# Kernel tuning notes

Measured on AMD Instinct MI355X. Metric: run time of the kernel, lower is better.

## Reference

```python
import jax, jax.numpy as jnp
import numpy as np

NUM_USERS = 100000
NUM_ITEMS = 50000
EMB_DIM = 128
N_EDGES = 1600000
BATCH = 16384
L_USER = (0, 1, 2)


def setup_inputs() -> dict:
    key = jax.random.key(0)
    k1, k2, k3, k4, k5, k6 = jax.random.split(key, 6)
    users = jax.random.randint(k1, (BATCH,), 0, NUM_USERS)
    items = jax.random.randint(k2, (BATCH,), 0, NUM_ITEMS)
    edge_src = jax.random.randint(k3, (N_EDGES,), 0, NUM_USERS)
    edge_dst = jax.random.randint(k4, (N_EDGES,), 0, NUM_USERS)
    # nn.Parameter init: normal(mean=0, std=0.01)
    user_emb = jax.random.normal(k5, (NUM_USERS, EMB_DIM), dtype=jnp.float32) * 0.01
    item_emb = jax.random.normal(k6, (NUM_ITEMS, EMB_DIM), dtype=jnp.float32) * 0.01
    return {"users": users, "items": items, "edge_src": edge_src,
            "edge_dst": edge_dst, "user_emb": user_emb, "item_emb": item_emb}


def social_conv(edge_src, edge_dst, h):
    # DGL copy_u -> mean aggregation over social (user-user) edges
    msgs = h[edge_src]  # [E, D] gather
    agg = jax.ops.segment_sum(msgs, edge_dst, num_segments=NUM_USERS)  # [N, D]
    deg = jax.ops.segment_sum(jnp.ones_like(edge_dst, dtype=h.dtype), edge_dst,
                              num_segments=NUM_USERS)  # [N]
    return agg / jnp.maximum(deg, 1.0)[:, None]


def reference(users, items, edge_src, edge_dst, user_emb, item_emb):
    g1 = social_conv(edge_src, edge_dst, user_emb)
    g2 = social_conv(edge_src, edge_dst, g1)
    final_user = jnp.zeros_like(user_emb)
    if 0 in L_USER:
        final_user = final_user + user_emb
    if 1 in L_USER:
        final_user = final_user + g1
    if 2 in L_USER:
        final_user = final_user + g2
    latest_user = final_user[users]   # [B, D]
    latest_item = item_emb[items]     # [B, D]
    predict = jax.nn.sigmoid(jnp.sum(latest_user * latest_item, axis=1))  # [B]
    return predict, latest_user, latest_item
```

## Files before the change

kernel.cpp:

```cpp
#include <hip/hip_runtime.h>
#include <math.h>

#define NUM_USERS 100000
#define NUM_ITEMS 50000
#define EMB_D 128
#define N_EDGES 1600000
#define BATCH 16384

#define NBINS 782
#define CHUNK 8192
#define NCHUNKS 196
#define CELL 40
#define CAP 64
#define BINSZ (NCHUNKS * CELL)

#define CVT_BLOCKS 3125

#define FP8_SCALE 512.0f
#define FP8_INV   (1.0f / 512.0f)

typedef unsigned int u32;
typedef unsigned char u8;
typedef float f32x2 __attribute__((ext_vector_type(2)));

__device__ __forceinline__ long long g18row(int u) {
    return (long long)(u >> 7) * BINSZ + (long long)(u & 127) * 32;
}

__global__ void prep_kernel(const float* __restrict__ in, u32* __restrict__ outp,
                            const int* __restrict__ edge_src, const int* __restrict__ edge_dst,
                            u32* __restrict__ coarse, u8* __restrict__ cellcnt) {
    __shared__ int cnt2[NBINS];
    int blk = blockIdx.x;
    int tid = threadIdx.x;
    if (blk >= NCHUNKS) {
        long long bbase = (long long)(blk - NCHUNKS) * 1024;
        float4 a[4];
        #pragma unroll
        for (int g = 0; g < 4; g++) a[g] = ((const float4*)in)[bbase + g * 256 + tid];
        #pragma unroll
        for (int g = 0; g < 4; g++) {
            int r = __builtin_amdgcn_cvt_pk_fp8_f32(a[g].x * FP8_SCALE, a[g].y * FP8_SCALE, 0, false);
            r = __builtin_amdgcn_cvt_pk_fp8_f32(a[g].z * FP8_SCALE, a[g].w * FP8_SCALE, r, true);
            outp[bbase + g * 256 + tid] = (u32)r;
        }
        return;
    }
    long long c0 = (long long)blk * CHUNK;
    int n = (int)min((long long)CHUNK, (long long)N_EDGES - c0);
    for (int i = tid; i < NBINS; i += 256) cnt2[i] = 0;
    __syncthreads();
    int n4 = n >> 2;
    const int4* d4p = (const int4*)(edge_dst + c0);
    const int4* s4p = (const int4*)(edge_src + c0);
    for (int i = tid; i < n4; i += 256) {
        int4 d = d4p[i];
        int4 s = s4p[i];
        int dd[4] = {d.x, d.y, d.z, d.w};
        int ss[4] = {s.x, s.y, s.z, s.w};
        #pragma unroll
        for (int k = 0; k < 4; k++) {
            int b = dd[k] >> 7;
            int idx = atomicAdd(&cnt2[b], 1);
            if (idx < CELL)
                coarse[(long long)b * BINSZ + blk * CELL + idx] =
                    ((u32)ss[k] << 7) | (u32)(dd[k] & 127);
        }
    }
    __syncthreads();
    for (int i = tid; i < NBINS; i += 256)
        cellcnt[(long long)blk * NBINS + i] = (u8)min(cnt2[i], CELL);
}

__global__ void binagg_kernel(u32* __restrict__ coarse, const u8* __restrict__ cellcnt,
                              const u32* __restrict__ tab32,
                              int* __restrict__ srt, int* __restrict__ counts) {
    __shared__ int cur[128];
    __shared__ int stage[128 * 65];
    int b = blockIdx.x;
    int tid = threadIdx.x;
    if (tid < 128) cur[tid] = 0;
    __syncthreads();
    long long cb = (long long)b * BINSZ;
    for (int i = tid; i < BINSZ; i += 512) {
        int cell = i / CELL;
        int slot = i - cell * CELL;
        if (slot < (int)cellcnt[(long long)cell * NBINS + b]) {
            u32 p = coarse[cb + i];
            int dl = (int)(p & 127u);
            int pos = atomicAdd(&cur[dl], 1);
            if (pos < CAP) stage[dl * 65 + pos] = (int)(p >> 7);
        }
    }
    __syncthreads();
    int binBase = b << 7;
    int wv = tid >> 6;
    int lane = tid & 63;
    int dlane = lane & 31;
    int hi = lane >> 5;
    for (int dl = wv; dl < 128; dl += 8) {
        int user = binBase + dl;
        if (user >= NUM_USERS) continue;
        int cnt = cur[dl];
        int cl = min(cnt, CAP);
        int sbase = dl * 65;
        float4 acc = make_float4(0.f, 0.f, 0.f, 0.f);
        int j = 0;
        for (; j + 16 <= cl; j += 16) {
            int rr[8];
            #pragma unroll
            for (int k = 0; k < 8; k++) {
                int s0 = stage[sbase + j + 2 * k];
                int s1 = stage[sbase + j + 2 * k + 1];
                rr[k] = hi ? s1 : s0;
            }
            u32 pp[8];
            #pragma unroll
            for (int k = 0; k < 8; k++) pp[k] = tab32[(long long)rr[k] * 32 + dlane];
            #pragma unroll
            for (int k = 0; k < 8; k++) {
                f32x2 d0 = __builtin_amdgcn_cvt_pk_f32_fp8((int)pp[k], false);
                f32x2 d1 = __builtin_amdgcn_cvt_pk_f32_fp8((int)pp[k], true);
                acc.x += d0.x; acc.y += d0.y; acc.z += d1.x; acc.w += d1.y;
            }
        }
        if (j < cl) {
            int rr[8]; float ww[8];
            #pragma unroll
            for (int k = 0; k < 8; k++) {
                int i0 = min(j + 2 * k, cl - 1);
                int i1 = min(j + 2 * k + 1, cl - 1);
                int s0 = stage[sbase + i0];
                int s1 = stage[sbase + i1];
                rr[k] = hi ? s1 : s0;
                ww[k] = ((j + 2 * k + hi) < cl) ? 1.0f : 0.0f;
            }
            u32 pp[8];
            #pragma unroll
            for (int k = 0; k < 8; k++) pp[k] = tab32[(long long)rr[k] * 32 + dlane];
            #pragma unroll
            for (int k = 0; k < 8; k++) {
                f32x2 d0 = __builtin_amdgcn_cvt_pk_f32_fp8((int)pp[k], false);
                f32x2 d1 = __builtin_amdgcn_cvt_pk_f32_fp8((int)pp[k], true);
                acc.x += d0.x * ww[k]; acc.y += d0.y * ww[k];
                acc.z += d1.x * ww[k]; acc.w += d1.y * ww[k];
            }
        }
        acc.x += __shfl_xor(acc.x, 32, 64);
        acc.y += __shfl_xor(acc.y, 32, 64);
        acc.z += __shfl_xor(acc.z, 32, 64);
        acc.w += __shfl_xor(acc.w, 32, 64);
        float inv = 1.0f / fmaxf((float)cnt, 1.0f);
        int enc = __builtin_amdgcn_cvt_pk_fp8_f32(acc.x * inv, acc.y * inv, 0, false);
        enc = __builtin_amdgcn_cvt_pk_fp8_f32(acc.z * inv, acc.w * inv, enc, true);
        if (lane < 32) coarse[g18row(user) + dlane] = (u32)enc;
        srt[(long long)user * CAP + lane] = stage[sbase + lane];
        if (lane == 0) counts[user] = cnt;
    }
}

__global__ void final_kernel(const int* __restrict__ users, const int* __restrict__ items,
                             const float* __restrict__ user_emb, const float* __restrict__ item_emb,
                             const u32* __restrict__ g18, const int* __restrict__ counts,
                             const int* __restrict__ srt,
                             float* __restrict__ out_predict, float* __restrict__ out_lu,
                             float* __restrict__ out_li) {
    int b = (blockIdx.x * blockDim.x + threadIdx.x) >> 6;
    int lane = threadIdx.x & 63;
    if (b >= BATCH) return;
    b = __builtin_amdgcn_readfirstlane(b);
    int u = users[b];
    int it = items[b];
    int cnt = counts[u];
    int cl = min(cnt, CAP);
    long long start = (long long)u * CAP;
    int dlane = lane & 31;
    int hi = lane >> 5;
    float4 acc = make_float4(0.f, 0.f, 0.f, 0.f);
    int j = 0;
    for (; j + 16 <= cl; j += 16) {
        int rr[8];
        #pragma unroll
        for (int k = 0; k < 8; k++) {
            int s0 = srt[start + j + 2 * k];
            int s1 = srt[start + j + 2 * k + 1];
            rr[k] = hi ? s1 : s0;
        }
        u32 pp[8];
        #pragma unroll
        for (int k = 0; k < 8; k++) pp[k] = g18[g18row(rr[k]) + dlane];
        #pragma unroll
        for (int k = 0; k < 8; k++) {
            f32x2 d0 = __builtin_amdgcn_cvt_pk_f32_fp8((int)pp[k], false);
            f32x2 d1 = __builtin_amdgcn_cvt_pk_f32_fp8((int)pp[k], true);
            acc.x += d0.x; acc.y += d0.y; acc.z += d1.x; acc.w += d1.y;
        }
    }
    if (j < cl) {
        int rr[8]; float ww[8];
        #pragma unroll
        for (int k = 0; k < 8; k++) {
            int i0 = min(j + 2 * k, cl - 1);
            int i1 = min(j + 2 * k + 1, cl - 1);
            int s0 = srt[start + i0];
            int s1 = srt[start + i1];
            rr[k] = hi ? s1 : s0;
            ww[k] = ((j + 2 * k + hi) < cl) ? 1.0f : 0.0f;
        }
        u32 pp[8];
        #pragma unroll
        for (int k = 0; k < 8; k++) pp[k] = g18[g18row(rr[k]) + dlane];
        #pragma unroll
        for (int k = 0; k < 8; k++) {
            f32x2 d0 = __builtin_amdgcn_cvt_pk_f32_fp8((int)pp[k], false);
            f32x2 d1 = __builtin_amdgcn_cvt_pk_f32_fp8((int)pp[k], true);
            acc.x += d0.x * ww[k]; acc.y += d0.y * ww[k];
            acc.z += d1.x * ww[k]; acc.w += d1.y * ww[k];
        }
    }
    acc.x += __shfl_xor(acc.x, 32, 64);
    acc.y += __shfl_xor(acc.y, 32, 64);
    acc.z += __shfl_xor(acc.z, 32, 64);
    acc.w += __shfl_xor(acc.w, 32, 64);
    float inv = (1.0f / fmaxf((float)cnt, 1.0f)) * FP8_INV;
    float4 ue = *(const float4*)(user_emb + (long long)u * EMB_D + dlane * 4);
    u32 a1p = g18[g18row(u) + dlane];
    f32x2 a0 = __builtin_amdgcn_cvt_pk_f32_fp8((int)a1p, false);
    f32x2 a1 = __builtin_amdgcn_cvt_pk_f32_fp8((int)a1p, true);
    float4 ie = *(const float4*)(item_emb + (long long)it * EMB_D + dlane * 4);
    float4 lu;
    lu.x = ue.x + a0.x * FP8_INV + acc.x * inv;
    lu.y = ue.y + a0.y * FP8_INV + acc.y * inv;
    lu.z = ue.z + a1.x * FP8_INV + acc.z * inv;
    lu.w = ue.w + a1.y * FP8_INV + acc.w * inv;
    if (lane < 32) {
        *(float4*)(out_lu + (long long)b * EMB_D + dlane * 4) = lu;
        *(float4*)(out_li + (long long)b * EMB_D + dlane * 4) = ie;
    }
    float dot = lu.x * ie.x + lu.y * ie.y + lu.z * ie.z + lu.w * ie.w;
    #pragma unroll
    for (int off = 16; off > 0; off >>= 1) dot += __shfl_down(dot, off, 64);
    if (lane == 0) out_predict[b] = 1.0f / (1.0f + expf(-dot));
}

extern "C" void kernel_launch(void* const* d_in, const int* in_sizes, int n_in,
                              void* d_out, int out_size, void* d_ws, size_t ws_size,
                              hipStream_t stream) {
    const int* users     = (const int*)d_in[0];
    const int* items     = (const int*)d_in[1];
    const int* edge_src  = (const int*)d_in[2];
    const int* edge_dst  = (const int*)d_in[3];
    const float* user_emb = (const float*)d_in[4];
    const float* item_emb = (const float*)d_in[5];

    const long long COARSE_U32 = (long long)NBINS * BINSZ;

    int* ws_i = (int*)d_ws;
    int* counts = ws_i;
    int* srt    = counts + 100352;
    u32* ue8    = (u32*)(srt + (long long)NUM_USERS * CAP);
    u32* coarse = ue8 + 3200000;
    u8*  cellcnt = (u8*)(coarse + COARSE_U32);

    float* out_predict = (float*)d_out;
    float* out_lu = out_predict + BATCH;
    float* out_li = out_lu + (long long)BATCH * EMB_D;

    prep_kernel<<<NCHUNKS + CVT_BLOCKS, 256, 0, stream>>>(
        user_emb, ue8, edge_src, edge_dst, coarse, cellcnt);

    binagg_kernel<<<NBINS, 512, 0, stream>>>(coarse, cellcnt, ue8, srt, counts);

    final_kernel<<<(BATCH + 3) / 4, 256, 0, stream>>>(
        users, items, user_emb, item_emb, coarse, counts, srt,
        out_predict, out_lu, out_li);
}
```

Measured before the change: 232.3 us.

## Stage edge partition cells in LDS with sentinels and write srt only for batch users

Splits the prep kernel into a separate fp8 conversion kernel (which also builds a bitmap of batch users) and a partition kernel that fills per-bin cells in LDS. Cells are pre-filled with a sentinel and then written to global memory as full uint4 rows. This removes the per-cell count array and the scattered 4-byte global writes, and lets binagg read coarse with vector loads and skip sentinels. binagg now writes the srt neighbour list only for users that appear in the batch, which cuts global write traffic. The cost is an extra memset and kernel launch, plus a partition kernel using about 128KB of dynamic LDS, which limits occupancy to one block per CU.

Measured after the change: 210.6 us. -9.4%, faster.

```diff
diff --git a/kernel.cpp b/kernel.cpp
--- a/kernel.cpp
+++ b/kernel.cpp
@@ -13,47 +13,61 @@
 #define CELL 40
 #define CAP 64
 #define BINSZ (NCHUNKS * CELL)
+#define SENT 0xFFFFFFFFu
 
 #define CVT_BLOCKS 3125
+#define BMAP_BLOCKS 64
 
 #define FP8_SCALE 512.0f
 #define FP8_INV   (1.0f / 512.0f)
 
 typedef unsigned int u32;
-typedef unsigned char u8;
 typedef float f32x2 __attribute__((ext_vector_type(2)));
 
 __device__ __forceinline__ long long g18row(int u) {
     return (long long)(u >> 7) * BINSZ + (long long)(u & 127) * 32;
 }
 
-__global__ void prep_kernel(const float* __restrict__ in, u32* __restrict__ outp,
-                            const int* __restrict__ edge_src, const int* __restrict__ edge_dst,
-                            u32* __restrict__ coarse, u8* __restrict__ cellcnt) {
-    __shared__ int cnt2[NBINS];
+__global__ void cvt_kernel(const float* __restrict__ in, u32* __restrict__ outp,
+                           const int* __restrict__ users, u32* __restrict__ bitmap) {
     int blk = blockIdx.x;
     int tid = threadIdx.x;
-    if (blk >= NCHUNKS) {
-        long long bbase = (long long)(blk - NCHUNKS) * 1024;
-        float4 a[4];
-        #pragma unroll
-        for (int g = 0; g < 4; g++) a[g] = ((const float4*)in)[bbase + g * 256 + tid];
-        #pragma unroll
-        for (int g = 0; g < 4; g++) {
-            int r = __builtin_amdgcn_cvt_pk_fp8_f32(a[g].x * FP8_SCALE, a[g].y * FP8_SCALE, 0, false);
-            r = __builtin_amdgcn_cvt_pk_fp8_f32(a[g].z * FP8_SCALE, a[g].w * FP8_SCALE, r, true);
-            outp[bbase + g * 256 + tid] = (u32)r;
+    if (blk >= CVT_BLOCKS) {
+        int i = (blk - CVT_BLOCKS) * 256 + tid;
+        if (i < BATCH) {
+            int u = users[i];
+            atomicOr(&bitmap[u >> 5], 1u << (u & 31));
         }
         return;
     }
+    long long bbase = (long long)blk * 1024;
+    float4 a[4];
+    #pragma unroll
+    for (int g = 0; g < 4; g++) a[g] = ((const float4*)in)[bbase + g * 256 + tid];
+    #pragma unroll
+    for (int g = 0; g < 4; g++) {
+        int r = __builtin_amdgcn_cvt_pk_fp8_f32(a[g].x * FP8_SCALE, a[g].y * FP8_SCALE, 0, false);
+        r = __builtin_amdgcn_cvt_pk_fp8_f32(a[g].z * FP8_SCALE, a[g].w * FP8_SCALE, r, true);
+        outp[bbase + g * 256 + tid] = (u32)r;
+    }
+}
+
+__global__ void part_kernel(const int* __restrict__ edge_src, const int* __restrict__ edge_dst,
+                            u32* __restrict__ coarse) {
+    extern __shared__ u32 sm[];
+    u32* cells = sm;
+    int* cnt2  = (int*)(sm + NBINS * CELL);
+    int blk = blockIdx.x;
+    int tid = threadIdx.x;
+    for (int i = tid; i < NBINS * CELL; i += 512) cells[i] = SENT;
+    for (int i = tid; i < NBINS; i += 512) cnt2[i] = 0;
+    __syncthreads();
     long long c0 = (long long)blk * CHUNK;
     int n = (int)min((long long)CHUNK, (long long)N_EDGES - c0);
-    for (int i = tid; i < NBINS; i += 256) cnt2[i] = 0;
-    __syncthreads();
     int n4 = n >> 2;
     const int4* d4p = (const int4*)(edge_dst + c0);
     const int4* s4p = (const int4*)(edge_src + c0);
-    for (int i = tid; i < n4; i += 256) {
+    for (int i = tid; i < n4; i += 512) {
         int4 d = d4p[i];
         int4 s = s4p[i];
         int dd[4] = {d.x, d.y, d.z, d.w};
@@ -63,17 +77,21 @@
             int b = dd[k] >> 7;
             int idx = atomicAdd(&cnt2[b], 1);
             if (idx < CELL)
-                coarse[(long long)b * BINSZ + blk * CELL + idx] =
-                    ((u32)ss[k] << 7) | (u32)(dd[k] & 127);
+                cells[b * CELL + idx] = ((u32)ss[k] << 7) | (u32)(dd[k] & 127);
         }
     }
     __syncthreads();
-    for (int i = tid; i < NBINS; i += 256)
-        cellcnt[(long long)blk * NBINS + i] = (u8)min(cnt2[i], CELL);
-}
-
-__global__ void binagg_kernel(u32* __restrict__ coarse, const u8* __restrict__ cellcnt,
-                              const u32* __restrict__ tab32,
+    const int I4 = NBINS * (CELL / 4);
+    for (int i4 = tid; i4 < I4; i4 += 512) {
+        int bin = i4 / (CELL / 4);
+        int off = i4 - bin * (CELL / 4);
+        *(uint4*)(coarse + (long long)bin * BINSZ + blk * CELL + off * 4) =
+            ((const uint4*)cells)[i4];
+    }
+}
+
+__global__ void binagg_kernel(u32* __restrict__ coarse, const u32* __restrict__ tab32,
+                              const u32* __restrict__ bitmap,
                               int* __restrict__ srt, int* __restrict__ counts) {
     __shared__ int cur[128];
     __shared__ int stage[128 * 65];
@@ -81,15 +99,18 @@
     int tid = threadIdx.x;
     if (tid < 128) cur[tid] = 0;
     __syncthreads();
-    long long cb = (long long)b * BINSZ;
-    for (int i = tid; i < BINSZ; i += 512) {
-        int cell = i / CELL;
-        int slot = i - cell * CELL;
-        if (slot < (int)cellcnt[(long long)cell * NBINS + b]) {
-            u32 p = coarse[cb + i];
-            int dl = (int)(p & 127u);
-            int pos = atomicAdd(&cur[dl], 1);
-            if (pos < CAP) stage[dl * 65 + pos] = (int)(p >> 7);
+    const uint4* col = (const uint4*)(coarse + (long long)b * BINSZ);
+    for (int i4 = tid; i4 < BINSZ / 4; i4 += 512) {
+        uint4 q = col[i4];
+        u32 pv[4] = {q.x, q.y, q.z, q.w};
+        #pragma unroll
+        for (int k = 0; k < 4; k++) {
+            u32 p = pv[k];
+            if (p != SENT) {
+                int dl = (int)(p & 127u);
+                int pos = atomicAdd(&cur[dl], 1);
+                if (pos < CAP) stage[dl * 65 + pos] = (int)(p >> 7);
+            }
         }
     }
     __syncthreads();
@@ -154,7 +175,8 @@
         int enc = __builtin_amdgcn_cvt_pk_fp8_f32(acc.x * inv, acc.y * inv, 0, false);
         enc = __builtin_amdgcn_cvt_pk_fp8_f32(acc.z * inv, acc.w * inv, enc, true);
         if (lane < 32) coarse[g18row(user) + dlane] = (u32)enc;
-        srt[(long long)user * CAP + lane] = stage[sbase + lane];
+        if ((bitmap[user >> 5] >> (user & 31)) & 1u)
+            srt[(long long)user * CAP + lane] = stage[sbase + lane];
         if (lane == 0) counts[user] = cnt;
     }
 }
@@ -254,22 +276,33 @@
     const float* item_emb = (const float*)d_in[5];
 
     const long long COARSE_U32 = (long long)NBINS * BINSZ;
+    const int SMEM_PART = (NBINS * CELL + NBINS) * 4;
 
     int* ws_i = (int*)d_ws;
     int* counts = ws_i;
     int* srt    = counts + 100352;
     u32* ue8    = (u32*)(srt + (long long)NUM_USERS * CAP);
     u32* coarse = ue8 + 3200000;
-    u8*  cellcnt = (u8*)(coarse + COARSE_U32);
+    u32* bitmap = coarse + COARSE_U32;
 
     float* out_predict = (float*)d_out;
     float* out_lu = out_predict + BATCH;
     float* out_li = out_lu + (long long)BATCH * EMB_D;
 
-    prep_kernel<<<NCHUNKS + CVT_BLOCKS, 256, 0, stream>>>(
-        user_emb, ue8, edge_src, edge_dst, coarse, cellcnt);
-
-    binagg_kernel<<<NBINS, 512, 0, stream>>>(coarse, cellcnt, ue8, srt, counts);
+    static int lds_set = 0;
+    if (!lds_set) {
+        hipFuncSetAttribute((const void*)part_kernel,
+                            hipFuncAttributeMaxDynamicSharedMemorySize, SMEM_PART);
+        lds_set = 1;
+    }
+
+    hipMemsetAsync(bitmap, 0, 3200 * sizeof(u32), stream);
+
+    cvt_kernel<<<CVT_BLOCKS + BMAP_BLOCKS, 256, 0, stream>>>(user_emb, ue8, users, bitmap);
+
+    part_kernel<<<NCHUNKS, 512, SMEM_PART, stream>>>(edge_src, edge_dst, coarse);
+
+    binagg_kernel<<<NBINS, 512, 0, stream>>>(coarse, ue8, bitmap, srt, counts);
 
     final_kernel<<<(BATCH + 3) / 4, 256, 0, stream>>>(
         users, items, user_emb, item_emb, coarse, counts, srt,
```
